# Kernel tuning notes

Measured on AMD Instinct MI355X. Metric: run time of the kernel, lower is better.

Reference implementation:

```python
import jax, jax.numpy as jnp
import numpy as np

B, N, F, D, KVQ, H, S, ITERS = 64, 4096, 256, 256, 256, 4, 8, 3
DH = KVQ // H
SCALE = DH ** -0.5
EPS = 1e-8
LN_EPS = 1e-5


def layernorm(x, w, b):
    m = jnp.mean(x, axis=-1, keepdims=True)
    v = jnp.var(x, axis=-1, keepdims=True)
    return (x - m) * jax.lax.rsqrt(v + LN_EPS) * w + b


def setup_inputs() -> dict:
    key = jax.random.key(0)
    ks = jax.random.split(key, 8)
    def init(k, shape, fan_in):
        return jax.random.normal(k, shape, dtype=jnp.float32) * (fan_in ** -0.5)
    return {
        "inputs": jax.random.normal(ks[0], (B, N, F), dtype=jnp.float32),
        "conditioning": jax.random.normal(ks[1], (B, S, D), dtype=jnp.float32),
        "ln_in_w": jnp.ones((F,), jnp.float32),
        "ln_in_b": jnp.zeros((F,), jnp.float32),
        "ln_s_w": jnp.ones((D,), jnp.float32),
        "ln_s_b": jnp.zeros((D,), jnp.float32),
        "wq": init(ks[2], (KVQ, D), D),
        "wk": init(ks[3], (KVQ, F), F),
        "wv": init(ks[4], (KVQ, F), F),
        "gru_wih": init(ks[5], (3 * D, KVQ), KVQ),
        "gru_whh": init(ks[6], (3 * D, D), D),
        "gru_bih": jnp.zeros((3 * D,), jnp.float32),
        "gru_bhh": jnp.zeros((3 * D,), jnp.float32),
    }


def gru_cell(x, h, wih, whh, bih, bhh):
    # x: [..., KVQ], h: [..., D]; torch.nn.GRUCell math
    gi = x @ wih.T + bih  # [..., 3D]
    gh = h @ whh.T + bhh
    i_r, i_z, i_n = jnp.split(gi, 3, axis=-1)
    h_r, h_z, h_n = jnp.split(gh, 3, axis=-1)
    r = jax.nn.sigmoid(i_r + h_r)
    z = jax.nn.sigmoid(i_z + h_z)
    n = jnp.tanh(i_n + r * h_n)
    return (1.0 - z) * n + z * h


def reference(inputs, conditioning, ln_in_w, ln_in_b, ln_s_w, ln_s_b, wq, wk, wv, gru_wih, gru_whh, gru_bih, gru_bhh):
    x = layernorm(inputs, ln_in_w, ln_in_b)  # [B,N,F]
    k = (x @ wk.T).reshape(B, N, H, DH)
    v = (x @ wv.T).reshape(B, N, H, DH)

    slots = conditioning
    attn_out = None
    for _ in range(ITERS):
        slots_prev = slots
        sn = layernorm(slots, ln_s_w, ln_s_b)
        q = (sn @ wq.T).reshape(B, S, H, DH)
        dots = jnp.einsum('bihd,bjhd->bihj', q, k) * SCALE  # [B,S,H,N]
        # inverted softmax: normalize over flattened (slot, head) axis
        attn = jax.nn.softmax(dots.reshape(B, S * H, N), axis=1).reshape(B, S, H, N)
        attn_before = attn
        attn = attn + EPS
        attn = attn / jnp.sum(attn, axis=-1, keepdims=True)
        updates = jnp.einsum('bjhd,bihj->bihd', v, attn).reshape(B, S, KVQ)
        slots = gru_cell(updates.reshape(-1, KVQ), slots_prev.reshape(-1, D),
                         gru_wih, gru_whh, gru_bih, gru_bhh).reshape(B, S, D)
        attn_out = jnp.mean(attn_before, axis=2)  # [B,S,N]
    return slots, attn_out
```

## Files before the change

kernel.cpp:

```cpp
#include <hip/hip_runtime.h>
#include <hip/hip_bf16.h>
#include <math.h>


using frag_ab = __attribute__((ext_vector_type(8))) short;
using f32x4  = __attribute__((ext_vector_type(4))) float;

__device__ __forceinline__ unsigned short f2bf(float f) {
  unsigned int x = __float_as_uint(f);
  x += 0x7fffu + ((x >> 16) & 1u);
  return (unsigned short)(x >> 16);
}
__device__ __forceinline__ float bf2f(unsigned short u) {
  return __uint_as_float((unsigned int)u << 16);
}

__global__ __launch_bounds__(256) void k_precvt(
    const float* __restrict__ xsrc, const float* __restrict__ lnw,
    const float* __restrict__ lnb, unsigned short* __restrict__ Xh) {
  const int lane = threadIdx.x & 63;
  const long row = (long)blockIdx.x * 4 + (threadIdx.x >> 6);
  const float4 v = *(const float4*)(xsrc + row * 256 + lane * 4);
  float s = v.x + v.y + v.z + v.w;
  float ss = v.x * v.x + v.y * v.y + v.z * v.z + v.w * v.w;
#pragma unroll
  for (int m = 1; m < 64; m <<= 1) {
    s += __shfl_xor(s, m);
    ss += __shfl_xor(ss, m);
  }
  const float mean = s * (1.f / 256.f);
  const float rstd = rsqrtf(ss * (1.f / 256.f) - mean * mean + 1e-5f);
  const float4 w4 = *(const float4*)(lnw + lane * 4);
  const float4 b4 = *(const float4*)(lnb + lane * 4);
  const float x0 = (v.x - mean) * rstd * w4.x + b4.x;
  const float x1 = (v.y - mean) * rstd * w4.y + b4.y;
  const float x2 = (v.z - mean) * rstd * w4.z + b4.z;
  const float x3 = (v.w - mean) * rstd * w4.w + b4.w;
  uint2 o;
  o.x = (unsigned)f2bf(x0) | ((unsigned)f2bf(x1) << 16);
  o.y = (unsigned)f2bf(x2) | ((unsigned)f2bf(x3) << 16);
  *(uint2*)(Xh + row * 256 + lane * 4) = o;
}

__global__ __launch_bounds__(256) void k_wcvt(const float* __restrict__ wk,
                                              const float* __restrict__ wv,
                                              unsigned short* __restrict__ Wb) {
  const int lane = threadIdx.x & 63;
  const int n = blockIdx.x * 4 + (threadIdx.x >> 6);
  const float* W = (n < 256) ? (wk + n * 256) : (wv + (long)(n - 256) * 256);
  const float4 w4 = *(const float4*)(W + lane * 4);
  uint2 o;
  o.x = (unsigned)f2bf(w4.x) | ((unsigned)f2bf(w4.y) << 16);
  o.y = (unsigned)f2bf(w4.z) | ((unsigned)f2bf(w4.w) << 16);
  *(uint2*)(Wb + n * 256 + lane * 4) = o;
}

__global__ void k_transpose(const float* __restrict__ wih,
                            const float* __restrict__ whh,
                            const float* __restrict__ wqs,
                            float* __restrict__ wihT, float* __restrict__ whhT,
                            float* __restrict__ wqT) {
  const int idx = blockIdx.x * 256 + threadIdx.x;
  if (idx < 768 * 256) {
    const int g = idx >> 8, k = idx & 255;
    wihT[k * 768 + g] = wih[idx];
  } else if (idx < 2 * 768 * 256) {
    const int j = idx - 768 * 256;
    const int g = j >> 8, k = j & 255;
    whhT[k * 768 + g] = whh[j];
  } else {
    const int j = idx - 2 * 768 * 256;
    const int c = j >> 8, k = j & 255;
    wqT[k * 256 + c] = wqs[j];
  }
}

__global__ __launch_bounds__(256) void k_gemm(
    const unsigned short* __restrict__ Xh, const unsigned short* __restrict__ Wb,
    unsigned short* __restrict__ Kb, unsigned short* __restrict__ Vt) {
  __shared__ __align__(16) char sh[65536];
  const int t = threadIdx.x;
  const int id = blockIdx.x;
  const int work = (id & 7) * 1024 + (id >> 3);
  const int mblk = work >> 2, nblk = work & 3;
  const long row0 = (long)mblk * 128;
  const int n0 = nblk * 128;
  const int lane = t & 63, w = t >> 6;
  const int wm = w >> 1, wn = w & 1;
  const int li = lane & 15, kg = lane >> 4;

  f32x4 acc[4][4];
#pragma unroll
  for (int m = 0; m < 4; ++m)
#pragma unroll
    for (int n = 0; n < 4; ++n) acc[m][n] = (f32x4){0.f, 0.f, 0.f, 0.f};

  auto stage = [&](int buf, int ks) {
    char* As = sh + (buf << 15);
    char* Bs = As + 16384;
#pragma unroll
    for (int rnd = 0; rnd < 4; ++rnd) {
      const int o = rnd * 4096 + t * 16;
      const int r = o >> 7, kb = o & 127;
      __builtin_amdgcn_global_load_lds(
          (const unsigned int*)((const char*)Xh + (row0 + r) * 512 + ks * 128 + kb),
          (unsigned int*)(As + o), 16, 0, 0);
      __builtin_amdgcn_global_load_lds(
          (const unsigned int*)((const char*)Wb + (long)(n0 + r) * 512 + ks * 128 + kb),
          (unsigned int*)(Bs + o), 16, 0, 0);
    }
  };

  stage(0, 0);
  __syncthreads();
  for (int ks = 0; ks < 4; ++ks) {
    const int cur = ks & 1;
    if (ks < 3) stage(cur ^ 1, ks + 1);
    const char* As = sh + (cur << 15);
    const char* Bs = As + 16384;
#pragma unroll
    for (int kk = 0; kk < 2; ++kk) {
      frag_ab af[4], bf[4];
#pragma unroll
      for (int m = 0; m < 4; ++m)
        af[m] = *(const frag_ab*)(As + (wm * 64 + m * 16 + li) * 128 + kk * 64 + kg * 16);
#pragma unroll
      for (int n = 0; n < 4; ++n)
        bf[n] = *(const frag_ab*)(Bs + (wn * 64 + n * 16 + li) * 128 + kk * 64 + kg * 16);
#pragma unroll
      for (int m = 0; m < 4; ++m)
#pragma unroll
        for (int n = 0; n < 4; ++n)
          acc[m][n] =
              __builtin_amdgcn_mfma_f32_16x16x32_bf16(af[m], bf[n], acc[m][n], 0, 0, 0);
    }
    __syncthreads();
  }

  if (nblk < 2) {
    unsigned short* Krep = (unsigned short*)sh;
#pragma unroll
    for (int m = 0; m < 4; ++m)
#pragma unroll
      for (int n = 0; n < 4; ++n) {
        const int C = wn * 64 + n * 16 + li;
#pragma unroll
        for (int r = 0; r < 4; ++r) {
          const int R = wm * 64 + m * 16 + kg * 4 + r;
          const int off = (R * 256 + C * 2) ^ (((R >> 2) & 3) << 5);
          *(unsigned short*)((char*)Krep + off) = f2bf(acc[m][n][r]);
        }
      }
    __syncthreads();
#pragma unroll
    for (int p = 0; p < 8; ++p) {
      const int idx = p * 256 + t;
      const int R = idx >> 4, c = (idx & 15) * 16;
      const uint4 v =
          *(const uint4*)((char*)Krep + ((R * 256 + c) ^ (((R >> 2) & 3) << 5)));
      *(uint4*)(Kb + (row0 + R) * 256 + nblk * 128 + c / 2) = v;
    }
  } else {
    unsigned short* Vrep = (unsigned short*)sh;
#pragma unroll
    for (int m = 0; m < 4; ++m)
#pragma unroll
      for (int n = 0; n < 4; ++n) {
        const int dl = wn * 64 + n * 16 + li;
#pragma unroll
        for (int r = 0; r < 4; ++r) {
          const int R = wm * 64 + m * 16 + kg * 4 + r;
          const int off = dl * 256 + ((R * 2) ^ ((dl & 7) << 4));
          *(unsigned short*)((char*)Vrep + off) = f2bf(acc[m][n][r]);
        }
      }
    __syncthreads();
    const long b = row0 >> 12;
    const long jb = row0 & 4095;
#pragma unroll
    for (int p = 0; p < 8; ++p) {
      const int idx = p * 256 + t;
      const int dl = idx >> 4, c16 = idx & 15;
      const uint4 v = *(const uint4*)((char*)Vrep + dl * 256 +
                                      ((c16 * 16) ^ ((dl & 7) << 4)));
      const int dglob = (nblk - 2) * 128 + dl;
      *(uint4*)(Vt + ((long)(b * 256 + dglob)) * 4096 + jb + c16 * 8) = v;
    }
  }
}

__global__ __launch_bounds__(256) void k_q(
    const float* __restrict__ slots, const float* __restrict__ lnw,
    const float* __restrict__ lnb, const float* __restrict__ wqT,
    float* __restrict__ qout) {
  __shared__ float sl[8 * 256];
  __shared__ float mstat[8], rstat[8];
  const int b = blockIdx.x, t = threadIdx.x;
#pragma unroll
  for (int i = 0; i < 8; ++i) sl[i * 256 + t] = slots[b * 2048 + i * 256 + t];
  __syncthreads();
  if (t < 8) {
    float s = 0.f, ss = 0.f;
    for (int k = 0; k < 256; ++k) {
      const float x = sl[t * 256 + k];
      s += x;
      ss += x * x;
    }
    const float m = s * (1.f / 256.f);
    mstat[t] = m;
    rstat[t] = rsqrtf(ss * (1.f / 256.f) - m * m + 1e-5f);
  }
  __syncthreads();
  const float w = lnw[t], bb = lnb[t];
#pragma unroll
  for (int i = 0; i < 8; ++i)
    sl[i * 256 + t] = (sl[i * 256 + t] - mstat[i]) * rstat[i] * w + bb;
  __syncthreads();
  float acc[8] = {};
  for (int k = 0; k < 256; k += 4) {
    const float w0 = wqT[(k + 0) * 256 + t];
    const float w1 = wqT[(k + 1) * 256 + t];
    const float w2 = wqT[(k + 2) * 256 + t];
    const float w3 = wqT[(k + 3) * 256 + t];
#pragma unroll
    for (int i = 0; i < 8; ++i) {
      const float4 x4 = *(const float4*)(sl + i * 256 + k);
      acc[i] += x4.x * w0 + x4.y * w1 + x4.z * w2 + x4.w * w3;
    }
  }
#pragma unroll
  for (int i = 0; i < 8; ++i) qout[b * 2048 + i * 256 + t] = acc[i];
}

template <bool LAST, bool FIRST>
__global__ __launch_bounds__(256) void k_att(
    const float* __restrict__ qin, const unsigned short* __restrict__ Kb,
    const unsigned short* __restrict__ Vt, float* __restrict__ upart,
    float* __restrict__ svpart, float* __restrict__ rowsum_part,
    float* __restrict__ attn_out) {
  __shared__ __align__(16) unsigned short Qs[32 * 256];
  __shared__ __align__(16) unsigned short Ps[4][1024];
  __shared__ float ured[4][2048];
  __shared__ float wred[4][32];
  __shared__ float svred[4][256];
  const int t = threadIdx.x;
  const int lane = t & 63, wid = t >> 6;
  const int li = lane & 15, kg = lane >> 4;
  const int b = blockIdx.y;
  const long j0 = (long)blockIdx.x * 256 + wid * 64;

  {
    const int ihq = t >> 3;
    const int iq = ihq >> 2, hq = ihq & 3;
    const int kb0 = (t & 7) * 32;
    const bool nz = (kb0 >> 6) == hq;
#pragma unroll
    for (int u = 0; u < 4; ++u) {
      const int k0 = kb0 + u * 8;
      uint4 g = make_uint4(0u, 0u, 0u, 0u);
      if (nz) {
        const float* qp = qin + b * 2048 + iq * 256 + k0;
        g.x = (unsigned)f2bf(qp[0]) | ((unsigned)f2bf(qp[1]) << 16);
        g.y = (unsigned)f2bf(qp[2]) | ((unsigned)f2bf(qp[3]) << 16);
        g.z = (unsigned)f2bf(qp[4]) | ((unsigned)f2bf(qp[5]) << 16);
        g.w = (unsigned)f2bf(qp[6]) | ((unsigned)f2bf(qp[7]) << 16);
      }
      *(uint4*)((char*)Qs + ihq * 512 + ((k0 * 2) ^ ((ihq & 7) << 4))) = g;
    }
  }
  __syncthreads();

  float rsum0 = 0.f, rsum1 = 0.f;
  f32x4 pv[4][4];
#pragma unroll
  for (int h = 0; h < 4; ++h)
#pragma unroll
    for (int dt = 0; dt < 4; ++dt) pv[h][dt] = (f32x4){0.f, 0.f, 0.f, 0.f};
  float svl[16];
#pragma unroll
  for (int u = 0; u < 16; ++u) svl[u] = 0.f;

  unsigned short* Pw = Ps[wid];

  for (int ch = 0; ch < 2; ++ch) {
    const long jc = j0 + ch * 32;
    f32x4 dacc[2][2];
    dacc[0][0] = (f32x4){0.f, 0.f, 0.f, 0.f};
    dacc[0][1] = (f32x4){0.f, 0.f, 0.f, 0.f};
    dacc[1][0] = (f32x4){0.f, 0.f, 0.f, 0.f};
    dacc[1][1] = (f32x4){0.f, 0.f, 0.f, 0.f};
#pragma unroll
    for (int jsub = 0; jsub < 2; ++jsub) {
      frag_ab kf[8];
      const unsigned short* kp =
          Kb + ((long)b * 4096 + jc + jsub * 16 + li) * 256 + kg * 8;
#pragma unroll
      for (int ks = 0; ks < 8; ++ks) kf[ks] = *(const frag_ab*)(kp + ks * 32);
#pragma unroll
      for (int g = 0; g < 2; ++g) {
        const int ihb = g * 16 + li;
        const char* qrow = (const char*)Qs + ihb * 512;
        const int swz = (ihb & 7) << 4;
#pragma unroll
        for (int ks = 0; ks < 8; ++ks) {
          const frag_ab qf = *(const frag_ab*)(qrow + ((ks * 64 + kg * 16) ^ swz));
          dacc[jsub][g] = __builtin_amdgcn_mfma_f32_16x16x32_bf16(
              kf[ks], qf, dacc[jsub][g], 0, 0, 0);
        }
      }
    }
    float p[2][2][4];
#pragma unroll
    for (int jsub = 0; jsub < 2; ++jsub) {
#pragma unroll
      for (int r = 0; r < 4; ++r) {
        const float d0 = dacc[jsub][0][r] * 0.125f;
        const float d1 = dacc[jsub][1][r] * 0.125f;
        float mx = fmaxf(d0, d1);
        mx = fmaxf(mx, __shfl_xor(mx, 1));
        mx = fmaxf(mx, __shfl_xor(mx, 2));
        mx = fmaxf(mx, __shfl_xor(mx, 4));
        mx = fmaxf(mx, __shfl_xor(mx, 8));
        float e0 = __expf(d0 - mx), e1 = __expf(d1 - mx);
        float sm = e0 + e1;
        sm += __shfl_xor(sm, 1);
        sm += __shfl_xor(sm, 2);
        sm += __shfl_xor(sm, 4);
        sm += __shfl_xor(sm, 8);
        const float inv = 1.f / sm;
        e0 *= inv;
        e1 *= inv;
        p[jsub][0][r] = e0;
        p[jsub][1][r] = e1;
        rsum0 += e0;
        rsum1 += e1;
        if (LAST) {
          float s0 = e0 + __shfl_xor(e0, 1);
          s0 += __shfl_xor(s0, 2);
          float s1 = e1 + __shfl_xor(e1, 1);
          s1 += __shfl_xor(s1, 2);
          if ((li & 3) == 0) {
            const long jg = jc + jsub * 16 + kg * 4 + r;
            attn_out[((long)b * 8 + (li >> 2)) * 4096 + jg] = s0 * 0.25f;
            attn_out[((long)b * 8 + 4 + (li >> 2)) * 4096 + jg] = s1 * 0.25f;
          }
        }
      }
    }
    asm volatile("s_waitcnt lgkmcnt(0)" ::: "memory");
#pragma unroll
    for (int g = 0; g < 2; ++g) {
      const int ih = g * 16 + li;
      char* prow = (char*)Pw + ih * 64;
      const int swz = ((ih >> 2) & 3) << 4;
#pragma unroll
      for (int jsub = 0; jsub < 2; ++jsub)
#pragma unroll
        for (int rp = 0; rp < 2; ++rp) {
          const unsigned int pk =
              (unsigned)f2bf(p[jsub][g][2 * rp]) |
              ((unsigned)f2bf(p[jsub][g][2 * rp + 1]) << 16);
          const int jb = (jsub * 16 + kg * 4 + 2 * rp) * 2;
          *(unsigned int*)(prow + (jb ^ swz)) = pk;
        }
    }
    asm volatile("s_waitcnt lgkmcnt(0)" ::: "memory");
#pragma unroll
    for (int h = 0; h < 4; ++h) {
      const int ihr = (li & 7) * 4 + h;
      const frag_ab pa = *(const frag_ab*)(
          (const char*)Pw + ihr * 64 + ((kg * 16) ^ (((ihr >> 2) & 3) << 4)));
#pragma unroll
      for (int dt = 0; dt < 4; ++dt) {
        const frag_ab vf = *(const frag_ab*)(
            Vt + ((long)b * 256 + h * 64 + dt * 16 + li) * 4096 + jc + kg * 8);
        pv[h][dt] =
            __builtin_amdgcn_mfma_f32_16x16x32_bf16(pa, vf, pv[h][dt], 0, 0, 0);
        if (FIRST) {
          const unsigned short* vu = (const unsigned short*)&vf;
          float s = 0.f;
#pragma unroll
          for (int e = 0; e < 8; ++e) s += bf2f(vu[e]);
          svl[h * 4 + dt] += s;
        }
      }
    }
  }

  if (kg < 2) {
#pragma unroll
    for (int h = 0; h < 4; ++h)
#pragma unroll
      for (int dt = 0; dt < 4; ++dt)
#pragma unroll
        for (int r = 0; r < 4; ++r)
          ured[wid][(kg * 4 + r) * 256 + h * 64 + dt * 16 + li] = pv[h][dt][r];
  }
  rsum0 += __shfl_xor(rsum0, 16);
  rsum0 += __shfl_xor(rsum0, 32);
  rsum1 += __shfl_xor(rsum1, 16);
  rsum1 += __shfl_xor(rsum1, 32);
  if (lane < 16) {
    wred[wid][lane] = rsum0;
    wred[wid][16 + lane] = rsum1;
  }
  if (FIRST) {
#pragma unroll
    for (int u = 0; u < 16; ++u) {
      svl[u] += __shfl_xor(svl[u], 16);
      svl[u] += __shfl_xor(svl[u], 32);
    }
    if (lane < 16) {
#pragma unroll
      for (int h = 0; h < 4; ++h)
#pragma unroll
        for (int dt = 0; dt < 4; ++dt)
          svred[wid][h * 64 + dt * 16 + lane] = svl[h * 4 + dt];
    }
  }
  __syncthreads();
  const long pb = (long)blockIdx.x * 64 + b;
#pragma unroll
  for (int o = 0; o < 8; ++o) {
    const int idx = o * 256 + t;
    const int i = idx >> 8, d = idx & 255;
    upart[(pb * 8 + i) * 256 + d] = ured[0][i * 256 + d] + ured[1][i * 256 + d] +
                                    ured[2][i * 256 + d] + ured[3][i * 256 + d];
  }
  if (t < 32)
    rowsum_part[pb * 32 + t] = wred[0][t] + wred[1][t] + wred[2][t] + wred[3][t];
  if (FIRST)
    svpart[pb * 256 + t] = svred[0][t] + svred[1][t] + svred[2][t] + svred[3][t];
}

template <bool LAST>
__global__ __launch_bounds__(256) void k_gruq(
    const float* __restrict__ upart, const float* __restrict__ svpart,
    const float* __restrict__ rowsum_part, const float* __restrict__ wihT,
    const float* __restrict__ whhT, const float* __restrict__ bih,
    const float* __restrict__ bhh, const float* __restrict__ lnw,
    const float* __restrict__ lnb, const float* __restrict__ wqT,
    float* __restrict__ slots, float* __restrict__ qout,
    float* __restrict__ dout) {
  __shared__ float xl[8 * 256];
  __shared__ float hl[8 * 256];
  __shared__ float rs[32];
  __shared__ float mstat[8], rstat[8];
  const int t = threadIdx.x;
  const int b = blockIdx.x;
  if (t < 32) {
    float s2 = 0.f;
#pragma unroll
    for (int p = 0; p < 16; ++p) s2 += rowsum_part[((long)(p * 64 + b)) * 32 + t];
    rs[t] = 1.f / (s2 + 4096.f * 1e-8f);
  }
  float svs = 0.f;
#pragma unroll
  for (int p = 0; p < 16; ++p) svs += svpart[((long)(p * 64 + b)) * 256 + t];
  __syncthreads();
  const int hcol = t >> 6;
#pragma unroll
  for (int r = 0; r < 8; ++r) {
    float pp = 0.f;
#pragma unroll
    for (int p = 0; p < 16; ++p)
      pp += upart[(((long)(p * 64 + b)) * 8 + r) * 256 + t];
    xl[r * 256 + t] = (pp + 1e-8f * svs) * rs[r * 4 + hcol];
    hl[r * 256 + t] = slots[b * 2048 + r * 256 + t];
  }
  __syncthreads();
  float air[8] = {}, aiz[8] = {}, ain[8] = {};
  float ahr[8] = {}, ahz[8] = {}, ahn[8] = {};
  for (int k = 0; k < 256; k += 4) {
    float wir[4], wiz[4], win_[4], whr[4], whz[4], whn[4];
#pragma unroll
    for (int u = 0; u < 4; ++u) {
      wir[u] = wihT[(k + u) * 768 + t];
      wiz[u] = wihT[(k + u) * 768 + 256 + t];
      win_[u] = wihT[(k + u) * 768 + 512 + t];
      whr[u] = whhT[(k + u) * 768 + t];
      whz[u] = whhT[(k + u) * 768 + 256 + t];
      whn[u] = whhT[(k + u) * 768 + 512 + t];
    }
#pragma unroll
    for (int r = 0; r < 8; ++r) {
      const float4 x4 = *(const float4*)(xl + r * 256 + k);
      const float4 h4 = *(const float4*)(hl + r * 256 + k);
      air[r] += x4.x * wir[0] + x4.y * wir[1] + x4.z * wir[2] + x4.w * wir[3];
      aiz[r] += x4.x * wiz[0] + x4.y * wiz[1] + x4.z * wiz[2] + x4.w * wiz[3];
      ain[r] += x4.x * win_[0] + x4.y * win_[1] + x4.z * win_[2] + x4.w * win_[3];
      ahr[r] += h4.x * whr[0] + h4.y * whr[1] + h4.z * whr[2] + h4.w * whr[3];
      ahz[r] += h4.x * whz[0] + h4.y * whz[1] + h4.z * whz[2] + h4.w * whz[3];
      ahn[r] += h4.x * whn[0] + h4.y * whn[1] + h4.z * whn[2] + h4.w * whn[3];
    }
  }
  const float bir = bih[t], biz = bih[256 + t], bin_ = bih[512 + t];
  const float bhr = bhh[t], bhz = bhh[256 + t], bhn = bhh[512 + t];
  float hn[8];
#pragma unroll
  for (int r = 0; r < 8; ++r) {
    const float rr = 1.f / (1.f + __expf(-(air[r] + bir + ahr[r] + bhr)));
    const float zz = 1.f / (1.f + __expf(-(aiz[r] + biz + ahz[r] + bhz)));
    const float nn2 = tanhf(ain[r] + bin_ + rr * (ahn[r] + bhn));
    hn[r] = (1.f - zz) * nn2 + zz * hl[r * 256 + t];
    slots[b * 2048 + r * 256 + t] = hn[r];
    if (LAST) dout[b * 2048 + r * 256 + t] = hn[r];
  }
  if (LAST) return;
  __syncthreads();
#pragma unroll
  for (int r = 0; r < 8; ++r) xl[r * 256 + t] = hn[r];
  __syncthreads();
  if (t < 8) {
    float s = 0.f, ss = 0.f;
    for (int k = 0; k < 256; ++k) {
      const float x = xl[t * 256 + k];
      s += x;
      ss += x * x;
    }
    const float m = s * (1.f / 256.f);
    mstat[t] = m;
    rstat[t] = rsqrtf(ss * (1.f / 256.f) - m * m + 1e-5f);
  }
  __syncthreads();
  const float w = lnw[t], bb = lnb[t];
#pragma unroll
  for (int i = 0; i < 8; ++i)
    xl[i * 256 + t] = (xl[i * 256 + t] - mstat[i]) * rstat[i] * w + bb;
  __syncthreads();
  float acq[8] = {};
  for (int k = 0; k < 256; k += 4) {
    const float w0 = wqT[(k + 0) * 256 + t];
    const float w1 = wqT[(k + 1) * 256 + t];
    const float w2 = wqT[(k + 2) * 256 + t];
    const float w3 = wqT[(k + 3) * 256 + t];
#pragma unroll
    for (int i = 0; i < 8; ++i) {
      const float4 x4 = *(const float4*)(xl + i * 256 + k);
      acq[i] += x4.x * w0 + x4.y * w1 + x4.z * w2 + x4.w * w3;
    }
  }
#pragma unroll
  for (int i = 0; i < 8; ++i) qout[b * 2048 + i * 256 + t] = acq[i];
}

extern "C" void kernel_launch(void* const* d_in, const int* in_sizes, int n_in,
                              void* d_out, int out_size, void* d_ws,
                              size_t ws_size, hipStream_t stream) {
  const float* xin = (const float*)d_in[0];
  const float* cond = (const float*)d_in[1];
  const float* lnin_w = (const float*)d_in[2];
  const float* lnin_b = (const float*)d_in[3];
  const float* lns_w = (const float*)d_in[4];
  const float* lns_b = (const float*)d_in[5];
  const float* wq = (const float*)d_in[6];
  const float* wk = (const float*)d_in[7];
  const float* wv = (const float*)d_in[8];
  const float* gwih = (const float*)d_in[9];
  const float* gwhh = (const float*)d_in[10];
  const float* gbih = (const float*)d_in[11];
  const float* gbhh = (const float*)d_in[12];
  float* out = (float*)d_out;

  char* ws = (char*)d_ws;
  unsigned short* Kb = (unsigned short*)ws;  ws += 64l * 4096 * 256 * 2;
  unsigned short* Vt = (unsigned short*)ws;  ws += 64l * 256 * 4096 * 2;
  unsigned short* Xh = (unsigned short*)ws;  ws += 262144l * 256 * 2;
  float* upart = (float*)ws;                 ws += 16l * 64 * 8 * 256 * 4;
  float* svpart = (float*)ws;                ws += 16l * 64 * 256 * 4;
  float* rowsum_part = (float*)ws;           ws += 16l * 64 * 32 * 4;
  float* qbuf = (float*)ws;                  ws += 512l * 256 * 4;
  float* slots = (float*)ws;                 ws += 512l * 256 * 4;
  float* wihT = (float*)ws;                  ws += 256l * 768 * 4;
  float* whhT = (float*)ws;                  ws += 256l * 768 * 4;
  float* wqT = (float*)ws;                   ws += 256l * 256 * 4;
  unsigned short* Wb = (unsigned short*)ws;  ws += 512l * 256 * 2;

  hipMemcpyAsync(slots, cond, 512 * 256 * 4, hipMemcpyDeviceToDevice, stream);
  k_wcvt<<<128, 256, 0, stream>>>(wk, wv, Wb);
  k_transpose<<<1792, 256, 0, stream>>>(gwih, gwhh, wq, wihT, whhT, wqT);
  k_precvt<<<65536, 256, 0, stream>>>(xin, lnin_w, lnin_b, Xh);
  k_gemm<<<8192, 256, 0, stream>>>(Xh, Wb, Kb, Vt);
  k_q<<<64, 256, 0, stream>>>(slots, lns_w, lns_b, wqT, qbuf);

  k_att<false, true><<<dim3(16, 64), 256, 0, stream>>>(
      qbuf, Kb, Vt, upart, svpart, rowsum_part, out + 131072);
  k_gruq<false><<<64, 256, 0, stream>>>(upart, svpart, rowsum_part, wihT, whhT,
                                        gbih, gbhh, lns_w, lns_b, wqT, slots,
                                        qbuf, out);
  k_att<false, false><<<dim3(16, 64), 256, 0, stream>>>(
      qbuf, Kb, Vt, upart, svpart, rowsum_part, out + 131072);
  k_gruq<false><<<64, 256, 0, stream>>>(upart, svpart, rowsum_part, wihT, whhT,
                                        gbih, gbhh, lns_w, lns_b, wqT, slots,
                                        qbuf, out);
  k_att<true, false><<<dim3(16, 64), 256, 0, stream>>>(
      qbuf, Kb, Vt, upart, svpart, rowsum_part, out + 131072);
  k_gruq<true><<<64, 256, 0, stream>>>(upart, svpart, rowsum_part, wihT, whhT,
                                       gbih, gbhh, lns_w, lns_b, wqT, slots,
                                       qbuf, out);
}
```

Measured before the change: 731.3 us.

## Fold Wq·Wk into per-head query map and apply Wv after attention

Drops the large K/V projection GEMM. Each head's Wq^T·Wk (with the scale) is precomputed, so queries act directly on the normalized inputs. Attention is taken against the normalized bf16 inputs and their transpose, and Wv is applied to the 32 small per-slot-head weighted input sums inside the GRU kernel. This removes writing and reading the 512 MB-scale K/V tensors, but the attention kernel now accumulates 256-wide feature outputs per head row, and the partial buffer and GRU work grow.

New measurement: 949.0 us. +29.8%, slower.

```diff
diff --git a/kernel.cpp b/kernel.cpp
--- a/kernel.cpp
+++ b/kernel.cpp
@@ -15,51 +15,11 @@
   return __uint_as_float((unsigned int)u << 16);
 }
 
-__global__ __launch_bounds__(256) void k_precvt(
-    const float* __restrict__ xsrc, const float* __restrict__ lnw,
-    const float* __restrict__ lnb, unsigned short* __restrict__ Xh) {
-  const int lane = threadIdx.x & 63;
-  const long row = (long)blockIdx.x * 4 + (threadIdx.x >> 6);
-  const float4 v = *(const float4*)(xsrc + row * 256 + lane * 4);
-  float s = v.x + v.y + v.z + v.w;
-  float ss = v.x * v.x + v.y * v.y + v.z * v.z + v.w * v.w;
-#pragma unroll
-  for (int m = 1; m < 64; m <<= 1) {
-    s += __shfl_xor(s, m);
-    ss += __shfl_xor(ss, m);
-  }
-  const float mean = s * (1.f / 256.f);
-  const float rstd = rsqrtf(ss * (1.f / 256.f) - mean * mean + 1e-5f);
-  const float4 w4 = *(const float4*)(lnw + lane * 4);
-  const float4 b4 = *(const float4*)(lnb + lane * 4);
-  const float x0 = (v.x - mean) * rstd * w4.x + b4.x;
-  const float x1 = (v.y - mean) * rstd * w4.y + b4.y;
-  const float x2 = (v.z - mean) * rstd * w4.z + b4.z;
-  const float x3 = (v.w - mean) * rstd * w4.w + b4.w;
-  uint2 o;
-  o.x = (unsigned)f2bf(x0) | ((unsigned)f2bf(x1) << 16);
-  o.y = (unsigned)f2bf(x2) | ((unsigned)f2bf(x3) << 16);
-  *(uint2*)(Xh + row * 256 + lane * 4) = o;
-}
-
-__global__ __launch_bounds__(256) void k_wcvt(const float* __restrict__ wk,
-                                              const float* __restrict__ wv,
-                                              unsigned short* __restrict__ Wb) {
-  const int lane = threadIdx.x & 63;
-  const int n = blockIdx.x * 4 + (threadIdx.x >> 6);
-  const float* W = (n < 256) ? (wk + n * 256) : (wv + (long)(n - 256) * 256);
-  const float4 w4 = *(const float4*)(W + lane * 4);
-  uint2 o;
-  o.x = (unsigned)f2bf(w4.x) | ((unsigned)f2bf(w4.y) << 16);
-  o.y = (unsigned)f2bf(w4.z) | ((unsigned)f2bf(w4.w) << 16);
-  *(uint2*)(Wb + n * 256 + lane * 4) = o;
-}
-
 __global__ void k_transpose(const float* __restrict__ wih,
                             const float* __restrict__ whh,
-                            const float* __restrict__ wqs,
+                            const float* __restrict__ wv,
                             float* __restrict__ wihT, float* __restrict__ whhT,
-                            float* __restrict__ wqT) {
+                            float* __restrict__ wvT) {
   const int idx = blockIdx.x * 256 + threadIdx.x;
   if (idx < 768 * 256) {
     const int g = idx >> 8, k = idx & 255;
@@ -71,131 +31,106 @@
   } else {
     const int j = idx - 2 * 768 * 256;
     const int c = j >> 8, k = j & 255;
-    wqT[k * 256 + c] = wqs[j];
-  }
-}
-
-__global__ __launch_bounds__(256) void k_gemm(
-    const unsigned short* __restrict__ Xh, const unsigned short* __restrict__ Wb,
-    unsigned short* __restrict__ Kb, unsigned short* __restrict__ Vt) {
-  __shared__ __align__(16) char sh[65536];
+    wvT[k * 256 + c] = wv[j];
+  }
+}
+
+__global__ __launch_bounds__(256) void k_mprep(const float* __restrict__ wq,
+                                               const float* __restrict__ wk,
+                                               float* __restrict__ M) {
+  const int D = blockIdx.x, h = blockIdx.y, f = threadIdx.x;
+  float acc = 0.f;
+#pragma unroll 8
+  for (int d = 0; d < 64; ++d)
+    acc += wq[(h * 64 + d) * 256 + D] * wk[(h * 64 + d) * 256 + f];
+  M[((h * 256) + D) * 256 + f] = acc * 0.125f;
+}
+
+__global__ __launch_bounds__(256) void k_precvt(
+    const float* __restrict__ xsrc, const float* __restrict__ lnw,
+    const float* __restrict__ lnb, unsigned short* __restrict__ Xh,
+    unsigned short* __restrict__ XhT) {
+  __shared__ __align__(16) unsigned short XT[256 * 68];
   const int t = threadIdx.x;
-  const int id = blockIdx.x;
-  const int work = (id & 7) * 1024 + (id >> 3);
-  const int mblk = work >> 2, nblk = work & 3;
-  const long row0 = (long)mblk * 128;
-  const int n0 = nblk * 128;
   const int lane = t & 63, w = t >> 6;
-  const int wm = w >> 1, wn = w & 1;
-  const int li = lane & 15, kg = lane >> 4;
-
-  f32x4 acc[4][4];
-#pragma unroll
-  for (int m = 0; m < 4; ++m)
-#pragma unroll
-    for (int n = 0; n < 4; ++n) acc[m][n] = (f32x4){0.f, 0.f, 0.f, 0.f};
-
-  auto stage = [&](int buf, int ks) {
-    char* As = sh + (buf << 15);
-    char* Bs = As + 16384;
-#pragma unroll
-    for (int rnd = 0; rnd < 4; ++rnd) {
-      const int o = rnd * 4096 + t * 16;
-      const int r = o >> 7, kb = o & 127;
-      __builtin_amdgcn_global_load_lds(
-          (const unsigned int*)((const char*)Xh + (row0 + r) * 512 + ks * 128 + kb),
-          (unsigned int*)(As + o), 16, 0, 0);
-      __builtin_amdgcn_global_load_lds(
-          (const unsigned int*)((const char*)Wb + (long)(n0 + r) * 512 + ks * 128 + kb),
-          (unsigned int*)(Bs + o), 16, 0, 0);
-    }
-  };
-
-  stage(0, 0);
-  __syncthreads();
-  for (int ks = 0; ks < 4; ++ks) {
-    const int cur = ks & 1;
-    if (ks < 3) stage(cur ^ 1, ks + 1);
-    const char* As = sh + (cur << 15);
-    const char* Bs = As + 16384;
-#pragma unroll
-    for (int kk = 0; kk < 2; ++kk) {
-      frag_ab af[4], bf[4];
-#pragma unroll
-      for (int m = 0; m < 4; ++m)
-        af[m] = *(const frag_ab*)(As + (wm * 64 + m * 16 + li) * 128 + kk * 64 + kg * 16);
-#pragma unroll
-      for (int n = 0; n < 4; ++n)
-        bf[n] = *(const frag_ab*)(Bs + (wn * 64 + n * 16 + li) * 128 + kk * 64 + kg * 16);
-#pragma unroll
-      for (int m = 0; m < 4; ++m)
-#pragma unroll
-        for (int n = 0; n < 4; ++n)
-          acc[m][n] =
-              __builtin_amdgcn_mfma_f32_16x16x32_bf16(af[m], bf[n], acc[m][n], 0, 0, 0);
-    }
-    __syncthreads();
-  }
-
-  if (nblk < 2) {
-    unsigned short* Krep = (unsigned short*)sh;
-#pragma unroll
-    for (int m = 0; m < 4; ++m)
-#pragma unroll
-      for (int n = 0; n < 4; ++n) {
-        const int C = wn * 64 + n * 16 + li;
-#pragma unroll
-        for (int r = 0; r < 4; ++r) {
-          const int R = wm * 64 + m * 16 + kg * 4 + r;
-          const int off = (R * 256 + C * 2) ^ (((R >> 2) & 3) << 5);
-          *(unsigned short*)((char*)Krep + off) = f2bf(acc[m][n][r]);
-        }
-      }
-    __syncthreads();
-#pragma unroll
-    for (int p = 0; p < 8; ++p) {
-      const int idx = p * 256 + t;
-      const int R = idx >> 4, c = (idx & 15) * 16;
-      const uint4 v =
-          *(const uint4*)((char*)Krep + ((R * 256 + c) ^ (((R >> 2) & 3) << 5)));
-      *(uint4*)(Kb + (row0 + R) * 256 + nblk * 128 + c / 2) = v;
-    }
-  } else {
-    unsigned short* Vrep = (unsigned short*)sh;
-#pragma unroll
-    for (int m = 0; m < 4; ++m)
-#pragma unroll
-      for (int n = 0; n < 4; ++n) {
-        const int dl = wn * 64 + n * 16 + li;
-#pragma unroll
-        for (int r = 0; r < 4; ++r) {
-          const int R = wm * 64 + m * 16 + kg * 4 + r;
-          const int off = dl * 256 + ((R * 2) ^ ((dl & 7) << 4));
-          *(unsigned short*)((char*)Vrep + off) = f2bf(acc[m][n][r]);
-        }
-      }
-    __syncthreads();
-    const long b = row0 >> 12;
-    const long jb = row0 & 4095;
-#pragma unroll
-    for (int p = 0; p < 8; ++p) {
-      const int idx = p * 256 + t;
-      const int dl = idx >> 4, c16 = idx & 15;
-      const uint4 v = *(const uint4*)((char*)Vrep + dl * 256 +
-                                      ((c16 * 16) ^ ((dl & 7) << 4)));
-      const int dglob = (nblk - 2) * 128 + dl;
-      *(uint4*)(Vt + ((long)(b * 256 + dglob)) * 4096 + jb + c16 * 8) = v;
-    }
+  const long row0 = (long)blockIdx.x * 64;
+  const long b = row0 >> 12;
+  const long j0 = row0 & 4095;
+
+  float w4[4], b4[4];
+#pragma unroll
+  for (int k = 0; k < 4; ++k) {
+    w4[k] = lnw[k * 64 + lane];
+    b4[k] = lnb[k * 64 + lane];
+  }
+  for (int rr = 0; rr < 16; ++rr) {
+    const long row = row0 + w * 16 + rr;
+    float x[4];
+    float s = 0.f, ss = 0.f;
+#pragma unroll
+    for (int k = 0; k < 4; ++k) {
+      x[k] = xsrc[row * 256 + k * 64 + lane];
+      s += x[k];
+      ss += x[k] * x[k];
+    }
+#pragma unroll
+    for (int m = 1; m < 64; m <<= 1) {
+      s += __shfl_xor(s, m);
+      ss += __shfl_xor(ss, m);
+    }
+    const float mean = s * (1.f / 256.f);
+    const float rstd = rsqrtf(ss * (1.f / 256.f) - mean * mean + 1e-5f);
+#pragma unroll
+    for (int k = 0; k < 4; ++k) {
+      const unsigned short u = f2bf((x[k] - mean) * rstd * w4[k] + b4[k]);
+      Xh[row * 256 + k * 64 + lane] = u;
+      *(unsigned short*)((char*)XT + (k * 64 + lane) * 136 + (w * 16 + rr) * 2) = u;
+    }
+  }
+  __syncthreads();
+#pragma unroll
+  for (int fp = 0; fp < 4; ++fp) {
+    const int f = fp * 64 + (t >> 2);
+    const int jq = t & 3;
+    uint2 v0 = *(const uint2*)((const char*)XT + f * 136 + jq * 32 + 0);
+    uint2 v1 = *(const uint2*)((const char*)XT + f * 136 + jq * 32 + 8);
+    uint2 v2 = *(const uint2*)((const char*)XT + f * 136 + jq * 32 + 16);
+    uint2 v3 = *(const uint2*)((const char*)XT + f * 136 + jq * 32 + 24);
+    unsigned short* dst = XhT + (b * 256 + f) * 4096 + j0 + jq * 16;
+    *(uint4*)(dst) = make_uint4(v0.x, v0.y, v1.x, v1.y);
+    *(uint4*)(dst + 8) = make_uint4(v2.x, v2.y, v3.x, v3.y);
+  }
+}
+
+__global__ __launch_bounds__(256) void k_sv(const unsigned short* __restrict__ XhT,
+                                            float* __restrict__ svx) {
+  const int b = blockIdx.x >> 2, fq = blockIdx.x & 3;
+  const int lane = threadIdx.x & 63, w = threadIdx.x >> 6;
+  for (int rr = 0; rr < 16; ++rr) {
+    const int f = fq * 64 + w * 16 + rr;
+    const unsigned short* p = XhT + ((long)(b * 256 + f)) * 4096;
+    float s = 0.f;
+#pragma unroll
+    for (int i = 0; i < 8; ++i) {
+      const uint4 v = *(const uint4*)(p + i * 512 + lane * 8);
+      s += bf2f((unsigned short)(v.x & 0xffff)) + bf2f((unsigned short)(v.x >> 16)) +
+           bf2f((unsigned short)(v.y & 0xffff)) + bf2f((unsigned short)(v.y >> 16)) +
+           bf2f((unsigned short)(v.z & 0xffff)) + bf2f((unsigned short)(v.z >> 16)) +
+           bf2f((unsigned short)(v.w & 0xffff)) + bf2f((unsigned short)(v.w >> 16));
+    }
+#pragma unroll
+    for (int m = 1; m < 64; m <<= 1) s += __shfl_xor(s, m);
+    if (lane == 0) svx[b * 256 + f] = s;
   }
 }
 
 __global__ __launch_bounds__(256) void k_q(
     const float* __restrict__ slots, const float* __restrict__ lnw,
-    const float* __restrict__ lnb, const float* __restrict__ wqT,
-    float* __restrict__ qout) {
+    const float* __restrict__ lnb, const float* __restrict__ M,
+    unsigned short* __restrict__ qt) {
   __shared__ float sl[8 * 256];
   __shared__ float mstat[8], rstat[8];
-  const int b = blockIdx.x, t = threadIdx.x;
+  const int b = blockIdx.x, h = blockIdx.y, t = threadIdx.x;
 #pragma unroll
   for (int i = 0; i < 8; ++i) sl[i * 256 + t] = slots[b * 2048 + i * 256 + t];
   __syncthreads();
@@ -217,71 +152,52 @@
     sl[i * 256 + t] = (sl[i * 256 + t] - mstat[i]) * rstat[i] * w + bb;
   __syncthreads();
   float acc[8] = {};
-  for (int k = 0; k < 256; k += 4) {
-    const float w0 = wqT[(k + 0) * 256 + t];
-    const float w1 = wqT[(k + 1) * 256 + t];
-    const float w2 = wqT[(k + 2) * 256 + t];
-    const float w3 = wqT[(k + 3) * 256 + t];
-#pragma unroll
-    for (int i = 0; i < 8; ++i) {
-      const float4 x4 = *(const float4*)(sl + i * 256 + k);
-      acc[i] += x4.x * w0 + x4.y * w1 + x4.z * w2 + x4.w * w3;
-    }
-  }
-#pragma unroll
-  for (int i = 0; i < 8; ++i) qout[b * 2048 + i * 256 + t] = acc[i];
-}
-
-template <bool LAST, bool FIRST>
+  const float* Mh = M + h * 65536;
+  for (int D = 0; D < 256; ++D) {
+    const float m = Mh[D * 256 + t];
+#pragma unroll
+    for (int i = 0; i < 8; ++i) acc[i] += sl[i * 256 + D] * m;
+  }
+#pragma unroll
+  for (int i = 0; i < 8; ++i) {
+    const int ih = i * 4 + h;
+    *(unsigned short*)((char*)qt + b * 16384 + ih * 512 +
+                       ((2 * t) ^ ((ih & 7) << 4))) = f2bf(acc[i]);
+  }
+}
+
+template <bool LAST>
 __global__ __launch_bounds__(256) void k_att(
-    const float* __restrict__ qin, const unsigned short* __restrict__ Kb,
-    const unsigned short* __restrict__ Vt, float* __restrict__ upart,
-    float* __restrict__ svpart, float* __restrict__ rowsum_part,
-    float* __restrict__ attn_out) {
+    const unsigned short* __restrict__ qt, const unsigned short* __restrict__ Xh,
+    const unsigned short* __restrict__ XhT, float* __restrict__ upart,
+    float* __restrict__ rowsum_part, float* __restrict__ attn_out) {
   __shared__ __align__(16) unsigned short Qs[32 * 256];
   __shared__ __align__(16) unsigned short Ps[4][1024];
   __shared__ float ured[4][2048];
   __shared__ float wred[4][32];
-  __shared__ float svred[4][256];
   const int t = threadIdx.x;
   const int lane = t & 63, wid = t >> 6;
   const int li = lane & 15, kg = lane >> 4;
   const int b = blockIdx.y;
   const long j0 = (long)blockIdx.x * 256 + wid * 64;
 
-  {
-    const int ihq = t >> 3;
-    const int iq = ihq >> 2, hq = ihq & 3;
-    const int kb0 = (t & 7) * 32;
-    const bool nz = (kb0 >> 6) == hq;
-#pragma unroll
-    for (int u = 0; u < 4; ++u) {
-      const int k0 = kb0 + u * 8;
-      uint4 g = make_uint4(0u, 0u, 0u, 0u);
-      if (nz) {
-        const float* qp = qin + b * 2048 + iq * 256 + k0;
-        g.x = (unsigned)f2bf(qp[0]) | ((unsigned)f2bf(qp[1]) << 16);
-        g.y = (unsigned)f2bf(qp[2]) | ((unsigned)f2bf(qp[3]) << 16);
-        g.z = (unsigned)f2bf(qp[4]) | ((unsigned)f2bf(qp[5]) << 16);
-        g.w = (unsigned)f2bf(qp[6]) | ((unsigned)f2bf(qp[7]) << 16);
-      }
-      *(uint4*)((char*)Qs + ihq * 512 + ((k0 * 2) ^ ((ihq & 7) << 4))) = g;
-    }
-  }
+#pragma unroll
+  for (int rnd = 0; rnd < 4; ++rnd)
+    __builtin_amdgcn_global_load_lds(
+        (const unsigned int*)((const char*)qt + b * 16384 + rnd * 4096 + t * 16),
+        (unsigned int*)((char*)Qs + rnd * 4096 + t * 16), 16, 0, 0);
   __syncthreads();
 
   float rsum0 = 0.f, rsum1 = 0.f;
-  f32x4 pv[4][4];
-#pragma unroll
-  for (int h = 0; h < 4; ++h)
-#pragma unroll
-    for (int dt = 0; dt < 4; ++dt) pv[h][dt] = (f32x4){0.f, 0.f, 0.f, 0.f};
-  float svl[16];
-#pragma unroll
-  for (int u = 0; u < 16; ++u) svl[u] = 0.f;
+  f32x4 pv[2][16];
+#pragma unroll
+  for (int s = 0; s < 2; ++s)
+#pragma unroll
+    for (int ft = 0; ft < 16; ++ft) pv[s][ft] = (f32x4){0.f, 0.f, 0.f, 0.f};
 
   unsigned short* Pw = Ps[wid];
 
+#pragma unroll
   for (int ch = 0; ch < 2; ++ch) {
     const long jc = j0 + ch * 32;
     f32x4 dacc[2][2];
@@ -293,14 +209,13 @@
     for (int jsub = 0; jsub < 2; ++jsub) {
       frag_ab kf[8];
       const unsigned short* kp =
-          Kb + ((long)b * 4096 + jc + jsub * 16 + li) * 256 + kg * 8;
+          Xh + ((long)b * 4096 + jc + jsub * 16 + li) * 256 + kg * 8;
 #pragma unroll
       for (int ks = 0; ks < 8; ++ks) kf[ks] = *(const frag_ab*)(kp + ks * 32);
 #pragma unroll
       for (int g = 0; g < 2; ++g) {
-        const int ihb = g * 16 + li;
-        const char* qrow = (const char*)Qs + ihb * 512;
-        const int swz = (ihb & 7) << 4;
+        const char* qrow = (const char*)Qs + (g * 16 + li) * 512;
+        const int swz = (li & 7) << 4;
 #pragma unroll
         for (int ks = 0; ks < 8; ++ks) {
           const frag_ab qf = *(const frag_ab*)(qrow + ((ks * 64 + kg * 16) ^ swz));
@@ -314,8 +229,8 @@
     for (int jsub = 0; jsub < 2; ++jsub) {
 #pragma unroll
       for (int r = 0; r < 4; ++r) {
-        const float d0 = dacc[jsub][0][r] * 0.125f;
-        const float d1 = dacc[jsub][1][r] * 0.125f;
+        const float d0 = dacc[jsub][0][r];
+        const float d1 = dacc[jsub][1][r];
         float mx = fmaxf(d0, d1);
         mx = fmaxf(mx, __shfl_xor(mx, 1));
         mx = fmaxf(mx, __shfl_xor(mx, 2));
@@ -365,37 +280,20 @@
         }
     }
     asm volatile("s_waitcnt lgkmcnt(0)" ::: "memory");
-#pragma unroll
-    for (int h = 0; h < 4; ++h) {
-      const int ihr = (li & 7) * 4 + h;
-      const frag_ab pa = *(const frag_ab*)(
-          (const char*)Pw + ihr * 64 + ((kg * 16) ^ (((ihr >> 2) & 3) << 4)));
-#pragma unroll
-      for (int dt = 0; dt < 4; ++dt) {
-        const frag_ab vf = *(const frag_ab*)(
-            Vt + ((long)b * 256 + h * 64 + dt * 16 + li) * 4096 + jc + kg * 8);
-        pv[h][dt] =
-            __builtin_amdgcn_mfma_f32_16x16x32_bf16(pa, vf, pv[h][dt], 0, 0, 0);
-        if (FIRST) {
-          const unsigned short* vu = (const unsigned short*)&vf;
-          float s = 0.f;
-#pragma unroll
-          for (int e = 0; e < 8; ++e) s += bf2f(vu[e]);
-          svl[h * 4 + dt] += s;
-        }
-      }
-    }
-  }
-
-  if (kg < 2) {
-#pragma unroll
-    for (int h = 0; h < 4; ++h)
-#pragma unroll
-      for (int dt = 0; dt < 4; ++dt)
-#pragma unroll
-        for (int r = 0; r < 4; ++r)
-          ured[wid][(kg * 4 + r) * 256 + h * 64 + dt * 16 + li] = pv[h][dt][r];
-  }
+    const frag_ab pa0 = *(const frag_ab*)(
+        (const char*)Pw + li * 64 + ((kg * 16) ^ (((li >> 2) & 3) << 4)));
+    const frag_ab pa1 = *(const frag_ab*)(
+        (const char*)Pw + (16 + li) * 64 +
+        ((kg * 16) ^ ((((16 + li) >> 2) & 3) << 4)));
+#pragma unroll
+    for (int ft = 0; ft < 16; ++ft) {
+      const frag_ab vf = *(const frag_ab*)(
+          XhT + ((long)b * 256 + ft * 16 + li) * 4096 + jc + kg * 8);
+      pv[0][ft] = __builtin_amdgcn_mfma_f32_16x16x32_bf16(pa0, vf, pv[0][ft], 0, 0, 0);
+      pv[1][ft] = __builtin_amdgcn_mfma_f32_16x16x32_bf16(pa1, vf, pv[1][ft], 0, 0, 0);
+    }
+  }
+
   rsum0 += __shfl_xor(rsum0, 16);
   rsum0 += __shfl_xor(rsum0, 32);
   rsum1 += __shfl_xor(rsum1, 16);
@@ -404,48 +302,41 @@
     wred[wid][lane] = rsum0;
     wred[wid][16 + lane] = rsum1;
   }
-  if (FIRST) {
-#pragma unroll
-    for (int u = 0; u < 16; ++u) {
-      svl[u] += __shfl_xor(svl[u], 16);
-      svl[u] += __shfl_xor(svl[u], 32);
-    }
-    if (lane < 16) {
-#pragma unroll
-      for (int h = 0; h < 4; ++h)
-#pragma unroll
-        for (int dt = 0; dt < 4; ++dt)
-          svred[wid][h * 64 + dt * 16 + lane] = svl[h * 4 + dt];
-    }
-  }
-  __syncthreads();
+
   const long pb = (long)blockIdx.x * 64 + b;
 #pragma unroll
-  for (int o = 0; o < 8; ++o) {
-    const int idx = o * 256 + t;
-    const int i = idx >> 8, d = idx & 255;
-    upart[(pb * 8 + i) * 256 + d] = ured[0][i * 256 + d] + ured[1][i * 256 + d] +
-                                    ured[2][i * 256 + d] + ured[3][i * 256 + d];
+  for (int p4 = 0; p4 < 4; ++p4) {
+    __syncthreads();
+    if ((kg >> 1) == (p4 & 1)) {
+#pragma unroll
+      for (int ft = 0; ft < 16; ++ft)
+#pragma unroll
+        for (int r = 0; r < 4; ++r)
+          ured[wid][((kg & 1) * 4 + r) * 256 + ft * 16 + li] = pv[p4 >> 1][ft][r];
+    }
+    __syncthreads();
+#pragma unroll
+    for (int o = 0; o < 8; ++o) {
+      const int idx = o * 256 + t;
+      upart[(pb * 32 + p4 * 8 + o) * 256 + t] =
+          ured[0][idx] + ured[1][idx] + ured[2][idx] + ured[3][idx];
+    }
   }
   if (t < 32)
     rowsum_part[pb * 32 + t] = wred[0][t] + wred[1][t] + wred[2][t] + wred[3][t];
-  if (FIRST)
-    svpart[pb * 256 + t] = svred[0][t] + svred[1][t] + svred[2][t] + svred[3][t];
 }
 
 template <bool LAST>
-__global__ __launch_bounds__(256) void k_gruq(
-    const float* __restrict__ upart, const float* __restrict__ svpart,
+__global__ __launch_bounds__(256) void k_gru(
+    const float* __restrict__ upart, const float* __restrict__ svx,
     const float* __restrict__ rowsum_part, const float* __restrict__ wihT,
-    const float* __restrict__ whhT, const float* __restrict__ bih,
-    const float* __restrict__ bhh, const float* __restrict__ lnw,
-    const float* __restrict__ lnb, const float* __restrict__ wqT,
-    float* __restrict__ slots, float* __restrict__ qout,
-    float* __restrict__ dout) {
+    const float* __restrict__ whhT, const float* __restrict__ wvT,
+    const float* __restrict__ bih, const float* __restrict__ bhh,
+    float* __restrict__ slots, float* __restrict__ dout) {
+  __shared__ float xu[32 * 256];
   __shared__ float xl[8 * 256];
   __shared__ float hl[8 * 256];
   __shared__ float rs[32];
-  __shared__ float mstat[8], rstat[8];
   const int t = threadIdx.x;
   const int b = blockIdx.x;
   if (t < 32) {
@@ -454,19 +345,29 @@
     for (int p = 0; p < 16; ++p) s2 += rowsum_part[((long)(p * 64 + b)) * 32 + t];
     rs[t] = 1.f / (s2 + 4096.f * 1e-8f);
   }
-  float svs = 0.f;
-#pragma unroll
-  for (int p = 0; p < 16; ++p) svs += svpart[((long)(p * 64 + b)) * 256 + t];
-  __syncthreads();
-  const int hcol = t >> 6;
-#pragma unroll
-  for (int r = 0; r < 8; ++r) {
+  __syncthreads();
+  const float svf = svx[b * 256 + t] * 1e-8f;
+#pragma unroll 4
+  for (int o = 0; o < 32; ++o) {
     float pp = 0.f;
 #pragma unroll
     for (int p = 0; p < 16; ++p)
-      pp += upart[(((long)(p * 64 + b)) * 8 + r) * 256 + t];
-    xl[r * 256 + t] = (pp + 1e-8f * svs) * rs[r * 4 + hcol];
-    hl[r * 256 + t] = slots[b * 2048 + r * 256 + t];
+      pp += upart[(((long)(p * 64 + b)) * 32 + o) * 256 + t];
+    xu[o * 256 + t] = (pp + svf) * rs[o];
+  }
+#pragma unroll
+  for (int r = 0; r < 8; ++r) hl[r * 256 + t] = slots[b * 2048 + r * 256 + t];
+  __syncthreads();
+  {
+    const int h = t >> 6;
+    float a8[8] = {};
+    for (int f = 0; f < 256; ++f) {
+      const float wv = wvT[f * 256 + t];
+#pragma unroll
+      for (int i = 0; i < 8; ++i) a8[i] += wv * xu[(i * 4 + h) * 256 + f];
+    }
+#pragma unroll
+    for (int i = 0; i < 8; ++i) xl[i * 256 + t] = a8[i];
   }
   __syncthreads();
   float air[8] = {}, aiz[8] = {}, ain[8] = {};
@@ -496,52 +397,15 @@
   }
   const float bir = bih[t], biz = bih[256 + t], bin_ = bih[512 + t];
   const float bhr = bhh[t], bhz = bhh[256 + t], bhn = bhh[512 + t];
-  float hn[8];
 #pragma unroll
   for (int r = 0; r < 8; ++r) {
     const float rr = 1.f / (1.f + __expf(-(air[r] + bir + ahr[r] + bhr)));
     const float zz = 1.f / (1.f + __expf(-(aiz[r] + biz + ahz[r] + bhz)));
     const float nn2 = tanhf(ain[r] + bin_ + rr * (ahn[r] + bhn));
-    hn[r] = (1.f - zz) * nn2 + zz * hl[r * 256 + t];
-    slots[b * 2048 + r * 256 + t] = hn[r];
-    if (LAST) dout[b * 2048 + r * 256 + t] = hn[r];
-  }
-  if (LAST) return;
-  __syncthreads();
-#pragma unroll
-  for (int r = 0; r < 8; ++r) xl[r * 256 + t] = hn[r];
-  __syncthreads();
-  if (t < 8) {
-    float s = 0.f, ss = 0.f;
-    for (int k = 0; k < 256; ++k) {
-      const float x = xl[t * 256 + k];
-      s += x;
-      ss += x * x;
-    }
-    const float m = s * (1.f / 256.f);
-    mstat[t] = m;
-    rstat[t] = rsqrtf(ss * (1.f / 256.f) - m * m + 1e-5f);
-  }
-  __syncthreads();
-  const float w = lnw[t], bb = lnb[t];
-#pragma unroll
-  for (int i = 0; i < 8; ++i)
-    xl[i * 256 + t] = (xl[i * 256 + t] - mstat[i]) * rstat[i] * w + bb;
-  __syncthreads();
-  float acq[8] = {};
-  for (int k = 0; k < 256; k += 4) {
-    const float w0 = wqT[(k + 0) * 256 + t];
-    const float w1 = wqT[(k + 1) * 256 + t];
-    const float w2 = wqT[(k + 2) * 256 + t];
-    const float w3 = wqT[(k + 3) * 256 + t];
-#pragma unroll
-    for (int i = 0; i < 8; ++i) {
-      const float4 x4 = *(const float4*)(xl + i * 256 + k);
-      acq[i] += x4.x * w0 + x4.y * w1 + x4.z * w2 + x4.w * w3;
-    }
-  }
-#pragma unroll
-  for (int i = 0; i < 8; ++i) qout[b * 2048 + i * 256 + t] = acq[i];
+    const float hn = (1.f - zz) * nn2 + zz * hl[r * 256 + t];
+    slots[b * 2048 + r * 256 + t] = hn;
+    if (LAST) dout[b * 2048 + r * 256 + t] = hn;
+  }
 }
 
 extern "C" void kernel_launch(void* const* d_in, const int* in_sizes, int n_in,
@@ -563,39 +427,37 @@
   float* out = (float*)d_out;
 
   char* ws = (char*)d_ws;
-  unsigned short* Kb = (unsigned short*)ws;  ws += 64l * 4096 * 256 * 2;
-  unsigned short* Vt = (unsigned short*)ws;  ws += 64l * 256 * 4096 * 2;
-  unsigned short* Xh = (unsigned short*)ws;  ws += 262144l * 256 * 2;
-  float* upart = (float*)ws;                 ws += 16l * 64 * 8 * 256 * 4;
-  float* svpart = (float*)ws;                ws += 16l * 64 * 256 * 4;
-  float* rowsum_part = (float*)ws;           ws += 16l * 64 * 32 * 4;
-  float* qbuf = (float*)ws;                  ws += 512l * 256 * 4;
-  float* slots = (float*)ws;                 ws += 512l * 256 * 4;
-  float* wihT = (float*)ws;                  ws += 256l * 768 * 4;
-  float* whhT = (float*)ws;                  ws += 256l * 768 * 4;
-  float* wqT = (float*)ws;                   ws += 256l * 256 * 4;
-  unsigned short* Wb = (unsigned short*)ws;  ws += 512l * 256 * 2;
+  unsigned short* Xh = (unsigned short*)ws;   ws += 262144l * 256 * 2;
+  unsigned short* XhT = (unsigned short*)ws;  ws += 64l * 256 * 4096 * 2;
+  float* M = (float*)ws;                      ws += 4l * 256 * 256 * 4;
+  unsigned short* qt = (unsigned short*)ws;   ws += 64l * 32 * 256 * 2;
+  float* upart = (float*)ws;                  ws += 16l * 64 * 32 * 256 * 4;
+  float* svx = (float*)ws;                    ws += 64l * 256 * 4;
+  float* rowsum_part = (float*)ws;            ws += 16l * 64 * 32 * 4;
+  float* slots = (float*)ws;                  ws += 512l * 256 * 4;
+  float* wihT = (float*)ws;                   ws += 256l * 768 * 4;
+  float* whhT = (float*)ws;                   ws += 256l * 768 * 4;
+  float* wvT = (float*)ws;                    ws += 256l * 256 * 4;
 
   hipMemcpyAsync(slots, cond, 512 * 256 * 4, hipMemcpyDeviceToDevice, stream);
-  k_wcvt<<<128, 256, 0, stream>>>(wk, wv, Wb);
-  k_transpose<<<1792, 256, 0, stream>>>(gwih, gwhh, wq, wihT, whhT, wqT);
-  k_precvt<<<65536, 256, 0, stream>>>(xin, lnin_w, lnin_b, Xh);
-  k_gemm<<<8192, 256, 0, stream>>>(Xh, Wb, Kb, Vt);
-  k_q<<<64, 256, 0, stream>>>(slots, lns_w, lns_b, wqT, qbuf);
-
-  k_att<false, true><<<dim3(16, 64), 256, 0, stream>>>(
-      qbuf, Kb, Vt, upart, svpart, rowsum_part, out + 131072);
-  k_gruq<false><<<64, 256, 0, stream>>>(upart, svpart, rowsum_part, wihT, whhT,
-                                        gbih, gbhh, lns_w, lns_b, wqT, slots,
-                                        qbuf, out);
-  k_att<false, false><<<dim3(16, 64), 256, 0, stream>>>(
-      qbuf, Kb, Vt, upart, svpart, rowsum_part, out + 131072);
-  k_gruq<false><<<64, 256, 0, stream>>>(upart, svpart, rowsum_part, wihT, whhT,
-                                        gbih, gbhh, lns_w, lns_b, wqT, slots,
-                                        qbuf, out);
-  k_att<true, false><<<dim3(16, 64), 256, 0, stream>>>(
-      qbuf, Kb, Vt, upart, svpart, rowsum_part, out + 131072);
-  k_gruq<true><<<64, 256, 0, stream>>>(upart, svpart, rowsum_part, wihT, whhT,
-                                       gbih, gbhh, lns_w, lns_b, wqT, slots,
-                                       qbuf, out);
-}
+  k_transpose<<<1792, 256, 0, stream>>>(gwih, gwhh, wv, wihT, whhT, wvT);
+  k_mprep<<<dim3(256, 4), 256, 0, stream>>>(wq, wk, M);
+  k_precvt<<<4096, 256, 0, stream>>>(xin, lnin_w, lnin_b, Xh, XhT);
+  k_sv<<<256, 256, 0, stream>>>(XhT, svx);
+
+  for (int it = 0; it < 3; ++it) {
+    k_q<<<dim3(64, 4), 256, 0, stream>>>(slots, lns_w, lns_b, M, qt);
+    if (it == 2)
+      k_att<true><<<dim3(16, 64), 256, 0, stream>>>(qt, Xh, XhT, upart,
+                                                    rowsum_part, out + 131072);
+    else
+      k_att<false><<<dim3(16, 64), 256, 0, stream>>>(qt, Xh, XhT, upart,
+                                                     rowsum_part, out + 131072);
+    if (it == 2)
+      k_gru<true><<<64, 256, 0, stream>>>(upart, svx, rowsum_part, wihT, whhT,
+                                          wvT, gbih, gbhh, slots, out);
+    else
+      k_gru<false><<<64, 256, 0, stream>>>(upart, svx, rowsum_part, wihT, whhT,
+                                           wvT, gbih, gbhh, slots, out);
+  }
+}
```
